# Kernel optimization log

Hardware: AMD Instinct MI355X
Metric: run time of the kernel (lower is better)

## Reference

```python
import jax, jax.numpy as jnp
import numpy as np
from jax import lax

B, N, C, T = 32, 1000, 32, 24
K, F_CHEB, F_TIME = 3, 64, 64


def setup_inputs() -> dict:
    key = jax.random.key(0)
    ks = jax.random.split(key, 7)
    return {
        "x": jax.random.normal(ks[0], (B, N, C, T), dtype=jnp.float32),
        "cheb_T": jax.random.normal(ks[1], (K, N, N), dtype=jnp.float32) * (1.0 / np.sqrt(N)),
        "Theta": jax.random.normal(ks[2], (K, C, F_CHEB), dtype=jnp.float32) * 0.1,
        "time_w": jax.random.normal(ks[3], (F_TIME, F_CHEB, 1, 3), dtype=jnp.float32) * 0.05,
        "time_b": jax.random.normal(ks[4], (F_TIME,), dtype=jnp.float32) * 0.05,
        "res_w": jax.random.normal(ks[5], (F_TIME, C, 1, 1), dtype=jnp.float32) * 0.1,
        "res_b": jax.random.normal(ks[6], (F_TIME,), dtype=jnp.float32) * 0.05,
    }


def _conv2d(x, w, stride_t, pad_t):
    # x: [B, Cin, N, T] (NCHW with H=nodes, W=time), w: [Cout, Cin, kh, kw]
    return lax.conv_general_dilated(
        x, w, window_strides=(1, stride_t), padding=((0, 0), (pad_t, pad_t)),
        dimension_numbers=("NCHW", "OIHW", "NCHW"))


def reference(x, cheb_T, Theta, time_w, time_b, res_w, res_b):
    # ChebConv: rhs_k[b,n,c,t] = sum_m T_k[m,n] x[b,m,c,t]; out = sum_k rhs_k @ Theta_k
    # Fused over all timesteps and polynomial orders in one einsum.
    spatial = jax.nn.relu(
        jnp.einsum("knm,bmct,kcf->bnft", cheb_T, x, Theta))  # [B,N,F_cheb,T]
    # time conv over the T axis (kernel (1,3), pad (0,1), stride (1,1))
    h = spatial.transpose(0, 2, 1, 3)  # [B,F_cheb,N,T]
    tc = _conv2d(h, time_w, 1, 1) + time_b[None, :, None, None]
    tc = jnp.tanh(tc) * jax.nn.sigmoid(tc)  # wave-net gating
    # 1x1 residual conv on the raw input (Dropout output in source is unused)
    res = _conv2d(x.transpose(0, 2, 1, 3), res_w, 1, 0) + res_b[None, :, None, None]
    out = (res + tc).transpose(0, 2, 1, 3)  # [B,N,F_time,T]
    return out
```

## Files before the change

### kernel.cpp

```cpp
#include <hip/hip_runtime.h>
#include <math.h>

typedef __attribute__((ext_vector_type(4))) float f32x4;
typedef __attribute__((ext_vector_type(16))) float f32x16;
typedef __attribute__((ext_vector_type(8))) short s16x8;
typedef __attribute__((ext_vector_type(8))) unsigned short u16x8;
typedef __attribute__((ext_vector_type(4))) unsigned short u16x4;

#define NB 32
#define NN 1000
#define NT 24
#define NP 1024
#define TCN 768

#define GLOAD16(g, l) __builtin_amdgcn_global_load_lds( \
    (const __attribute__((address_space(1))) unsigned int*)(g), \
    (__attribute__((address_space(3))) unsigned int*)(l), 16, 0, 0)

__device__ __forceinline__ unsigned short f2bf(float f){
  union { float fv; unsigned int u; } v; v.fv = f;
  unsigned int r = v.u + 0x7FFFu + ((v.u >> 16) & 1u);
  return (unsigned short)(r >> 16);
}

__global__ void k0_cheb(const float* __restrict__ cheb, unsigned short* __restrict__ cbT){
  int idx = blockIdx.x * 256 + threadIdx.x;
  int base = idx << 2;
  int m = base & (NP - 1);
  int r = base >> 10;
  int n = r & (NP - 1);
  int k = r >> 10;
  u16x4 o;
  #pragma unroll
  for (int i = 0; i < 4; ++i){
    int mm = m + i;
    float v = (n < NN && mm < NN) ? cheb[((long)k*NN + n)*NN + mm] : 0.f;
    o[i] = f2bf(v);
  }
  *(u16x4*)(cbT + base) = o;
}

__global__ __launch_bounds__(256) void k0_x(const float* __restrict__ x,
                     unsigned short* __restrict__ xbT, unsigned short* __restrict__ xt2){
  __shared__ unsigned short tile[64*770];
  const int b  = blockIdx.x >> 4;
  const int m0 = (blockIdx.x & 15) << 6;
  const int tid = threadIdx.x;
  for (int i = tid; i < 64*192; i += 256){
    int mi = i / 192, c4 = (i - mi*192) << 2;
    f32x4 v = (f32x4){0.f,0.f,0.f,0.f};
    if (m0 + mi < NN) v = *(const f32x4*)(x + (size_t)(b*NN + m0 + mi)*768 + c4);
    unsigned short* tp = tile + mi*770 + c4;
    tp[0] = f2bf(v[0]); tp[1] = f2bf(v[1]); tp[2] = f2bf(v[2]); tp[3] = f2bf(v[3]);
  }
  __syncthreads();
  {
    const int seg = tid & 7, r0 = tid >> 3;
    for (int rr = 0; rr < 768; rr += 32){
      int r = rr + r0;
      int t = r >> 5, c = r & 31, ct = c*24 + t;
      u16x8 v;
      #pragma unroll
      for (int e = 0; e < 8; ++e) v[e] = tile[(seg*8 + e)*770 + ct];
      *(u16x8*)(xbT + ((size_t)b*TCN + r)*NP + m0 + seg*8) = v;
    }
  }
  if (m0 < NN){
    int rows = NN - m0; if (rows > 64) rows = 64;
    for (int i = tid; i < rows*96; i += 256){
      int mi = i / 96, s = i - mi*96;
      u16x8 v;
      #pragma unroll
      for (int e = 0; e < 8; ++e){
        int r = s*8 + e; int t = r >> 5, c = r & 31;
        v[e] = tile[mi*770 + c*24 + t];
      }
      *(u16x8*)(xt2 + (size_t)(b*NN + m0 + mi)*TCN + s*8) = v;
    }
  }
}

__global__ void k0_w(const float* __restrict__ Theta, const float* __restrict__ tw,
                     const float* __restrict__ rw,
                     unsigned short* __restrict__ ThT, unsigned short* __restrict__ WtT,
                     unsigned short* __restrict__ rwT){
  int i = blockIdx.x * 256 + threadIdx.x;
  if (i < 64*96){
    int f = i / 96, kc = i - f*96;
    ThT[i] = f2bf(Theta[kc*64 + f]);
  }
  if (i < 64*192){
    int f = i / 192, kk = i - f*192;
    int dt = kk >> 6, fi = kk & 63;
    WtT[i] = f2bf(tw[(f*64 + fi)*3 + dt]);
  }
  if (i < 64*32){
    rwT[i] = f2bf(rw[i]);
  }
}

__global__ __launch_bounds__(256, 3) void k1_cheb_theta(
    const unsigned short* __restrict__ cbT,
    const unsigned short* __restrict__ xbT,
    const unsigned short* __restrict__ ThT,
    unsigned short* __restrict__ spa)
{
  __shared__ __align__(16) unsigned short smem[20480];

  int pB = blockIdx.x;
  int lb = (pB & 7) * 384 + (pB >> 3);
  const int tcb = lb % 6; lb /= 6;
  const int nt  = lb & 15;
  const int b   = lb >> 4;

  const int tid  = threadIdx.x;
  const int wid  = tid >> 6;
  const int lane = tid & 63;
  const int l31  = lane & 31;
  const int h    = lane >> 5;
  const int wr   = wid >> 1;
  const int wc   = wid & 1;

  const int rl4 = lane >> 2;
  const int swz = (((lane & 3) ^ ((rl4 >> 1) & 3)) << 3);
  const unsigned short* baseA = cbT + (size_t)(nt*64 + rl4)*NP + swz;
  const unsigned short* baseB = xbT + ((size_t)b*TCN + tcb*128 + rl4)*NP + swz;
  char* smc = (char*)smem;

  const int s_rd = (l31 >> 1) & 3;
  const int ch0 = ((h ^ s_rd) << 3);
  const int ch1 = (((2 + h) ^ s_rd) << 3);

  f32x16 acc[3][2];
  #pragma unroll
  for (int k = 0; k < 3; ++k)
    #pragma unroll
    for (int j = 0; j < 2; ++j)
      #pragma unroll
      for (int r = 0; r < 16; ++r) acc[k][j][r] = 0.f;

  const int rA  = wr*32 + l31;
  const int rB0 = wc*64 + l31;

  {
    #pragma unroll
    for (int q = 0; q < 5; ++q){
      const int g = wid*5 + q;
      if (g < 12){
        const int k = g >> 2, rg = g & 3;
        GLOAD16(baseA + (size_t)k*NP*NP + rg*16*NP, smc + k*4096 + rg*1024);
      } else {
        const int rg = g - 12;
        GLOAD16(baseB + (size_t)rg*16*NP, smc + 12288 + rg*1024);
      }
    }
  }
  __syncthreads();

  int cur = 0;
  for (int step = 0; step < 32; ++step){
    if (step < 31){
      const int so = (step + 1) << 5;
      const int bo = (cur ^ 1) * 20480;
      #pragma unroll
      for (int q = 0; q < 5; ++q){
        const int g = wid*5 + q;
        if (g < 12){
          const int k = g >> 2, rg = g & 3;
          GLOAD16(baseA + (size_t)k*NP*NP + rg*16*NP + so, smc + bo + k*4096 + rg*1024);
        } else {
          const int rg = g - 12;
          GLOAD16(baseB + (size_t)rg*16*NP + so, smc + bo + 12288 + rg*1024);
        }
      }
    }
    const unsigned short* sb = smem + cur*10240;
    #pragma unroll
    for (int ks = 0; ks < 2; ++ks){
      const int ch = ks ? ch1 : ch0;
      s16x8 bf0 = *(const s16x8*)(sb + 6144 + rB0*32 + ch);
      s16x8 bf1 = *(const s16x8*)(sb + 6144 + (rB0 + 32)*32 + ch);
      #pragma unroll
      for (int k = 0; k < 3; ++k){
        s16x8 af = *(const s16x8*)(sb + k*2048 + rA*32 + ch);
        acc[k][0] = __builtin_amdgcn_mfma_f32_32x32x16_bf16(af, bf0, acc[k][0], 0, 0, 0);
        acc[k][1] = __builtin_amdgcn_mfma_f32_32x32x16_bf16(af, bf1, acc[k][1], 0, 0, 0);
      }
    }
    __syncthreads();
    cur ^= 1;
  }

  s16x8 b2[3][2];
  const int fE = wc*32 + l31;
  #pragma unroll
  for (int ch = 0; ch < 3; ++ch)
    #pragma unroll
    for (int ks = 0; ks < 2; ++ks)
      b2[ch][ks] = *(const s16x8*)(ThT + fE*96 + ch*32 + ks*16 + h*8);

  unsigned short* yl = smem;
  const int rowE = wr*32 + l31;
  #pragma unroll
  for (int p = 0; p < 4; ++p){
    __syncthreads();
    if (wc == (p >> 1)){
      const int jj = p & 1;
      #pragma unroll
      for (int k = 0; k < 3; ++k)
        #pragma unroll
        for (int r = 0; r < 16; ++r){
          const int nl = wr*32 + (r & 3) + ((r >> 2) << 3) + (h << 2);
          const int kc = k*32 + l31;
          const int q  = kc >> 3;
          yl[nl*104 + (((q ^ (nl & 3)) << 3) | (kc & 7))] = f2bf(acc[k][jj][r]);
        }
    }
    __syncthreads();
    f32x16 a2c;
    #pragma unroll
    for (int r = 0; r < 16; ++r) a2c[r] = 0.f;
    #pragma unroll
    for (int ch = 0; ch < 3; ++ch)
      #pragma unroll
      for (int ks = 0; ks < 2; ++ks){
        const int q = ch*4 + ks*2 + h;
        s16x8 a2 = *(const s16x8*)(yl + rowE*104 + ((q ^ (rowE & 3)) << 3));
        a2c = __builtin_amdgcn_mfma_f32_32x32x16_bf16(a2, b2[ch][ks], a2c, 0, 0, 0);
      }
    const int t = tcb*4 + p;
    #pragma unroll
    for (int r = 0; r < 16; ++r){
      const int nl = wr*32 + (r & 3) + ((r >> 2) << 3) + (h << 2);
      const int n  = nt*64 + nl;
      if (n < NN)
        spa[((size_t)(b*NN + n)*NT + t)*64 + fE] = f2bf(fmaxf(a2c[r], 0.f));
    }
  }
}

__global__ __launch_bounds__(256, 3) void k2_out(
    const unsigned short* __restrict__ spa, const unsigned short* __restrict__ xt2,
    const unsigned short* __restrict__ WtT, const unsigned short* __restrict__ rwT,
    const float* __restrict__ tb, const float* __restrict__ rb,
    float* __restrict__ out)
{
  const int tid  = threadIdx.x;
  const int wid  = tid >> 6;
  const int lane = tid & 63;
  const int l16  = lane & 15;
  const int k8   = lane >> 4;
  const int gwave = blockIdx.x * 4 + wid;

  s16x8 bw[6][4], br[4];
  #pragma unroll
  for (int ch = 0; ch < 6; ++ch)
    #pragma unroll
    for (int j = 0; j < 4; ++j)
      bw[ch][j] = *(const s16x8*)(WtT + (j*16 + l16)*192 + ch*32 + k8*8);
  #pragma unroll
  for (int j = 0; j < 4; ++j)
    br[j] = *(const s16x8*)(rwT + (j*16 + l16)*32 + k8*8);
  float tbv[4], rbv[4];
  #pragma unroll
  for (int j = 0; j < 4; ++j){ tbv[j] = tb[j*16 + l16]; rbv[j] = rb[j*16 + l16]; }

  for (int it = 0; it < 4; ++it){
    const int r0 = gwave*64 + it*16;
    const int rowA = r0 + l16;
    const int tA = rowA % 24;
    const int bn = rowA / 24;
    f32x4 acc_tc[4], acc_res[4];
    #pragma unroll
    for (int j = 0; j < 4; ++j){ acc_tc[j] = (f32x4){0.f,0.f,0.f,0.f}; acc_res[j] = (f32x4){0.f,0.f,0.f,0.f}; }

    #pragma unroll
    for (int ch = 0; ch < 6; ++ch){
      const int dt = ch >> 1, fh = (ch & 1) << 5;
      const int ts = tA + dt - 1;
      s16x8 a = (s16x8){0,0,0,0,0,0,0,0};
      if (ts >= 0 && ts < 24)
        a = *(const s16x8*)(spa + ((size_t)(bn*24 + ts) << 6) + fh + k8*8);
      #pragma unroll
      for (int j = 0; j < 4; ++j)
        acc_tc[j] = __builtin_amdgcn_mfma_f32_16x16x32_bf16(a, bw[ch][j], acc_tc[j], 0, 0, 0);
    }
    {
      s16x8 a = *(const s16x8*)(xt2 + (size_t)bn*768 + tA*32 + k8*8);
      #pragma unroll
      for (int j = 0; j < 4; ++j)
        acc_res[j] = __builtin_amdgcn_mfma_f32_16x16x32_bf16(a, br[j], acc_res[j], 0, 0, 0);
    }

    const int rowD = r0 + (k8 << 2);
    const int tD  = rowD % 24;
    const int bnD = rowD / 24;
    #pragma unroll
    for (int j = 0; j < 4; ++j){
      f32x4 v;
      #pragma unroll
      for (int r = 0; r < 4; ++r){
        float z = acc_tc[j][r] + tbv[j];
        float e = __expf(-z);
        float p = (1.f - e) * __builtin_amdgcn_rcpf(1.f + e*e);
        v[r] = acc_res[j][r] + rbv[j] + p;
      }
      *(f32x4*)(out + (((size_t)bnD << 6) + j*16 + l16)*24 + tD) = v;
    }
  }
}

extern "C" void kernel_launch(void* const* d_in, const int* in_sizes, int n_in,
                              void* d_out, int out_size, void* d_ws, size_t ws_size,
                              hipStream_t stream) {
  const float* x     = (const float*)d_in[0];
  const float* cheb  = (const float*)d_in[1];
  const float* Theta = (const float*)d_in[2];
  const float* tw    = (const float*)d_in[3];
  const float* tb    = (const float*)d_in[4];
  const float* rw    = (const float*)d_in[5];
  const float* rb    = (const float*)d_in[6];
  float* out = (float*)d_out;

  char* ws = (char*)d_ws;
  size_t off = 0;
  auto alloc = [&](size_t bytes) -> void* {
    void* p = ws + off;
    off += (bytes + 255) & ~(size_t)255;
    return p;
  };
  unsigned short* cbT = (unsigned short*)alloc((size_t)3*NP*NP*2);
  unsigned short* xbT = (unsigned short*)alloc((size_t)NB*TCN*NP*2);
  unsigned short* xt2 = (unsigned short*)alloc((size_t)NB*NN*TCN*2);
  unsigned short* spa = (unsigned short*)alloc((size_t)NB*NN*NT*64*2);
  unsigned short* ThT = (unsigned short*)alloc((size_t)64*96*2);
  unsigned short* WtT = (unsigned short*)alloc((size_t)64*192*2);
  unsigned short* rwT = (unsigned short*)alloc((size_t)64*32*2);

  hipLaunchKernelGGL(k0_cheb, dim3(3072), dim3(256), 0, stream, cheb, cbT);
  hipLaunchKernelGGL(k0_x,    dim3(512),  dim3(256), 0, stream, x, xbT, xt2);
  hipLaunchKernelGGL(k0_w,    dim3(48),   dim3(256), 0, stream, Theta, tw, rw, ThT, WtT, rwT);
  hipLaunchKernelGGL(k1_cheb_theta, dim3(32*16*6), dim3(256), 0, stream, cbT, xbT, ThT, spa);
  hipLaunchKernelGGL(k2_out,  dim3(3000), dim3(256), 0, stream, spa, xt2, WtT, rwT, tb, rb, out);
}
```

Measured before the change: 438.0 us.

## Rework output kernel to 32x32 MFMA with LDS-staged stores; vectorize cheb load

```diff
diff --git a/kernel.cpp b/kernel.cpp
--- a/kernel.cpp
+++ b/kernel.cpp
@@ -30,12 +30,16 @@
   int r = base >> 10;
   int n = r & (NP - 1);
   int k = r >> 10;
-  u16x4 o;
-  #pragma unroll
-  for (int i = 0; i < 4; ++i){
-    int mm = m + i;
-    float v = (n < NN && mm < NN) ? cheb[((long)k*NN + n)*NN + mm] : 0.f;
-    o[i] = f2bf(v);
+  u16x4 o = (u16x4){0,0,0,0};
+  if (n < NN && m < NN){
+    if (m + 3 < NN){
+      f32x4 v = *(const f32x4*)(cheb + ((size_t)k*NN + n)*NN + m);
+      o[0] = f2bf(v[0]); o[1] = f2bf(v[1]); o[2] = f2bf(v[2]); o[3] = f2bf(v[3]);
+    } else {
+      #pragma unroll
+      for (int i = 0; i < 4; ++i)
+        if (m + i < NN) o[i] = f2bf(cheb[((size_t)k*NN + n)*NN + m + i]);
+    }
   }
   *(u16x4*)(cbT + base) = o;
 }
@@ -239,73 +243,77 @@
   }
 }
 
-__global__ __launch_bounds__(256, 3) void k2_out(
+__global__ __launch_bounds__(512, 4) void k2_out(
     const unsigned short* __restrict__ spa, const unsigned short* __restrict__ xt2,
     const unsigned short* __restrict__ WtT, const unsigned short* __restrict__ rwT,
     const float* __restrict__ tb, const float* __restrict__ rb,
     float* __restrict__ out)
 {
+  __shared__ float ylds[8][64*33];
   const int tid  = threadIdx.x;
   const int wid  = tid >> 6;
   const int lane = tid & 63;
-  const int l16  = lane & 15;
-  const int k8   = lane >> 4;
-  const int gwave = blockIdx.x * 4 + wid;
-
-  s16x8 bw[6][4], br[4];
+  const int l31  = lane & 31;
+  const int h    = lane >> 5;
+  float* my = &ylds[wid][0];
+
+  const int wbase = (blockIdx.x * 8 + wid) * 96;
+  const float tb0 = tb[l31], tb1 = tb[32 + l31];
+  const float rb0 = rb[l31], rb1 = rb[32 + l31];
+
   #pragma unroll
-  for (int ch = 0; ch < 6; ++ch)
-    #pragma unroll
-    for (int j = 0; j < 4; ++j)
-      bw[ch][j] = *(const s16x8*)(WtT + (j*16 + l16)*192 + ch*32 + k8*8);
-  #pragma unroll
-  for (int j = 0; j < 4; ++j)
-    br[j] = *(const s16x8*)(rwT + (j*16 + l16)*32 + k8*8);
-  float tbv[4], rbv[4];
-  #pragma unroll
-  for (int j = 0; j < 4; ++j){ tbv[j] = tb[j*16 + l16]; rbv[j] = rb[j*16 + l16]; }
-
-  for (int it = 0; it < 4; ++it){
-    const int r0 = gwave*64 + it*16;
-    const int rowA = r0 + l16;
+  for (int g = 0; g < 3; ++g){
+    const int rg0  = wbase + g*32;
+    const int rowA = rg0 + l31;
     const int tA = rowA % 24;
     const int bn = rowA / 24;
-    f32x4 acc_tc[4], acc_res[4];
-    #pragma unroll
-    for (int j = 0; j < 4; ++j){ acc_tc[j] = (f32x4){0.f,0.f,0.f,0.f}; acc_res[j] = (f32x4){0.f,0.f,0.f,0.f}; }
-
-    #pragma unroll
-    for (int ch = 0; ch < 6; ++ch){
-      const int dt = ch >> 1, fh = (ch & 1) << 5;
+
+    f32x16 atc[2], ars[2];
+    #pragma unroll
+    for (int r = 0; r < 16; ++r){ atc[0][r]=0.f; atc[1][r]=0.f; ars[0][r]=0.f; ars[1][r]=0.f; }
+
+    #pragma unroll
+    for (int s = 0; s < 12; ++s){
+      const int dt = s >> 2;
       const int ts = tA + dt - 1;
       s16x8 a = (s16x8){0,0,0,0,0,0,0,0};
       if (ts >= 0 && ts < 24)
-        a = *(const s16x8*)(spa + ((size_t)(bn*24 + ts) << 6) + fh + k8*8);
-      #pragma unroll
-      for (int j = 0; j < 4; ++j)
-        acc_tc[j] = __builtin_amdgcn_mfma_f32_16x16x32_bf16(a, bw[ch][j], acc_tc[j], 0, 0, 0);
-    }
-    {
-      s16x8 a = *(const s16x8*)(xt2 + (size_t)bn*768 + tA*32 + k8*8);
-      #pragma unroll
-      for (int j = 0; j < 4; ++j)
-        acc_res[j] = __builtin_amdgcn_mfma_f32_16x16x32_bf16(a, br[j], acc_res[j], 0, 0, 0);
-    }
-
-    const int rowD = r0 + (k8 << 2);
-    const int tD  = rowD % 24;
-    const int bnD = rowD / 24;
-    #pragma unroll
-    for (int j = 0; j < 4; ++j){
-      f32x4 v;
-      #pragma unroll
-      for (int r = 0; r < 4; ++r){
-        float z = acc_tc[j][r] + tbv[j];
+        a = *(const s16x8*)(spa + ((size_t)(bn*24 + ts)) * 64 + (s & 3)*16 + h*8);
+      s16x8 b0 = *(const s16x8*)(WtT + (size_t)l31*192 + s*16 + h*8);
+      s16x8 b1 = *(const s16x8*)(WtT + (size_t)(32 + l31)*192 + s*16 + h*8);
+      atc[0] = __builtin_amdgcn_mfma_f32_32x32x16_bf16(a, b0, atc[0], 0, 0, 0);
+      atc[1] = __builtin_amdgcn_mfma_f32_32x32x16_bf16(a, b1, atc[1], 0, 0, 0);
+    }
+    #pragma unroll
+    for (int s = 0; s < 2; ++s){
+      s16x8 a = *(const s16x8*)(xt2 + (size_t)bn*768 + tA*32 + s*16 + h*8);
+      s16x8 b0 = *(const s16x8*)(rwT + (size_t)l31*32 + s*16 + h*8);
+      s16x8 b1 = *(const s16x8*)(rwT + (size_t)(32 + l31)*32 + s*16 + h*8);
+      ars[0] = __builtin_amdgcn_mfma_f32_32x32x16_bf16(a, b0, ars[0], 0, 0, 0);
+      ars[1] = __builtin_amdgcn_mfma_f32_32x32x16_bf16(a, b1, ars[1], 0, 0, 0);
+    }
+
+    #pragma unroll
+    for (int jn = 0; jn < 2; ++jn){
+      const float tbv = jn ? tb1 : tb0;
+      const float rbv = jn ? rb1 : rb0;
+      const int f = jn*32 + l31;
+      #pragma unroll
+      for (int r = 0; r < 16; ++r){
+        const int tl = (r & 3) + ((r >> 2) << 3) + (h << 2);
+        float z = atc[jn][r] + tbv;
         float e = __expf(-z);
         float p = (1.f - e) * __builtin_amdgcn_rcpf(1.f + e*e);
-        v[r] = acc_res[j][r] + rbv[j] + p;
-      }
-      *(f32x4*)(out + (((size_t)bnD << 6) + j*16 + l16)*24 + tD) = v;
+        my[f*33 + tl] = ars[jn][r] + rbv + p;
+      }
+    }
+    #pragma unroll
+    for (int c = 0; c < 8; ++c){
+      const int row = rg0 + c*4;
+      const int t   = row % 24;
+      const int bnw = row / 24;
+      f32x4 v = *(const f32x4*)(my + lane*33 + c*4);
+      *(f32x4*)(out + ((size_t)bnw*64 + lane)*24 + t) = v;
     }
   }
 }
@@ -341,5 +349,5 @@
   hipLaunchKernelGGL(k0_x,    dim3(512),  dim3(256), 0, stream, x, xbT, xt2);
   hipLaunchKernelGGL(k0_w,    dim3(48),   dim3(256), 0, stream, Theta, tw, rw, ThT, WtT, rwT);
   hipLaunchKernelGGL(k1_cheb_theta, dim3(32*16*6), dim3(256), 0, stream, cbT, xbT, ThT, spa);
-  hipLaunchKernelGGL(k2_out,  dim3(3000), dim3(256), 0, stream, spa, xt2, WtT, rwT, tb, rb, out);
-}
+  hipLaunchKernelGGL(k2_out,  dim3(1000), dim3(512), 0, stream, spa, xt2, WtT, rwT, tb, rb, out);
+}
```

After: 481.3 us. 1.1x slower.
